# Performance work log

Measured on AMD Instinct MI355X. Metric: run time of the kernel, lower is better.

Reference implementation:

```python
import jax, jax.numpy as jnp
import numpy as np

K = 4
V = 32000
H = 512
B = 16
SOS = 1
EOS = 2


def setup_inputs() -> dict:
    key = jax.random.key(0)
    ks = jax.random.split(key, 8)
    s = 0.08  # small init keeps GRU/log_softmax well-conditioned
    return {
        "enc_h": jax.random.normal(ks[0], (B, H), jnp.float32),
        "E": jax.random.normal(ks[1], (V, H), jnp.float32) * s,
        "W_ih": jax.random.normal(ks[2], (H, 3 * H), jnp.float32) * s,
        "W_hh": jax.random.normal(ks[3], (H, 3 * H), jnp.float32) * s,
        "b_ih": jax.random.normal(ks[4], (3 * H,), jnp.float32) * s,
        "b_hh": jax.random.normal(ks[5], (3 * H,), jnp.float32) * s,
        "Wo": jax.random.normal(ks[6], (H, V), jnp.float32) * s,
        "bo": jax.random.normal(ks[7], (V,), jnp.float32) * s,
        "max_length": 32,
    }


def _beam_search(enc_h, E, W_ih, W_hh, b_ih, b_hh, Wo, bo, T):
    BK = B * K
    pos = jnp.arange(B, dtype=jnp.int32) * K  # pos_index
    # torch .repeat beam inflation: tiled layout (index i -> original i % B)
    h0 = jnp.tile(enc_h, (K, 1))  # [BK, H]
    inp0 = jnp.full((BK,), SOS, dtype=jnp.int32)
    ss0 = jnp.full((BK,), -jnp.inf, dtype=enc_h.dtype).at[pos].set(0.0)

    def gru(x, h):
        gi = x @ W_ih + b_ih
        gh = h @ W_hh + b_hh
        ir, iz, inn = jnp.split(gi, 3, axis=-1)
        hr, hz, hn = jnp.split(gh, 3, axis=-1)
        r = jax.nn.sigmoid(ir + hr)
        z = jax.nn.sigmoid(iz + hz)
        n = jnp.tanh(inn + r * hn)
        return (1.0 - z) * n + z * h

    def fwd_step(carry, _):
        inp, h, ss = carry
        h_new = gru(E[inp], h)                                   # [BK, H]
        logp = jax.nn.log_softmax(h_new @ Wo + bo, axis=-1)      # [BK, V]
        total = (ss[:, None] + logp).reshape(B, K * V)
        scores, cand = jax.lax.top_k(total, K)                   # [B, K]
        symbols = (cand % V).astype(jnp.int32).reshape(-1)       # input_var
        preds = (cand // V + pos[:, None]).astype(jnp.int32).reshape(-1)
        h_sel = h_new[preds]                                     # index_select hidden
        ss_new = scores.reshape(-1)
        ss_masked = jnp.where(symbols == EOS, -jnp.inf, ss_new)  # EOS masking
        return (symbols, h_sel, ss_masked), (logp, ss_new, preds, symbols, h_sel)

    _, (logps, step_scores, preds, syms, hiddens) = jax.lax.scan(
        fwd_step, (inp0, h0, ss0), None, length=T)

    # ---------------- backtrack ----------------
    last = step_scores[-1].reshape(B, K)
    s0, sorted_idx = jax.lax.top_k(last, K)
    tpred0 = (sorted_idx.astype(jnp.int32) + pos[:, None]).reshape(-1)
    lens0 = jnp.full((B, K), T, dtype=jnp.int32)
    hn0 = jnp.zeros((BK, H), dtype=enc_h.dtype)
    eos0 = jnp.zeros((B,), dtype=jnp.int32)

    def bt_step(carry, xs):
        tpred, eosf, s, lens, hn = carry
        logp_t, hid_t, pred_t, sym_t, score_t, tt = xs
        cur_out = logp_t[tpred]
        cur_hid = hid_t[tpred]
        cur_sym = sym_t[tpred]
        new_pred = pred_t[tpred]
        eos = sym_t == EOS
        eos_bk = eos.reshape(B, K).astype(jnp.int32)
        # original loop processes eos hits in descending beam order per batch
        higher = jnp.cumsum(eos_bk[:, ::-1], axis=1)[:, ::-1] - eos_bk
        occ = eosf[:, None] + higher
        res_k = K - occ % K - 1
        res_flat = (pos[:, None] + res_k).reshape(-1)
        idx = jnp.where(eos, res_flat, BK)  # BK = out of bounds -> dropped
        new_pred = new_pred.at[idx].set(pred_t, mode='drop')
        cur_out = cur_out.at[idx].set(logp_t, mode='drop')
        cur_hid = cur_hid.at[idx].set(hid_t, mode='drop')
        hn = hn.at[idx].set(hid_t, mode='drop')
        cur_sym = cur_sym.at[idx].set(sym_t, mode='drop')
        s = s.reshape(-1).at[idx].set(score_t, mode='drop').reshape(B, K)
        lens = lens.reshape(-1).at[idx].set(tt + 1, mode='drop').reshape(B, K)
        eosf = eosf + eos_bk.sum(axis=1)
        return (new_pred, eosf, s, lens, hn), (cur_out, cur_sym)

    ts = jnp.arange(T - 1, -1, -1, dtype=jnp.int32)
    (_, _, s_fin, lens_fin, hn_fin), (outs_rev, syms_rev) = jax.lax.scan(
        bt_step, (tpred0, eos0, s0, lens0, hn0),
        (logps[::-1], hiddens[::-1], preds[::-1], syms[::-1], step_scores[::-1], ts))

    s_sorted, re_idx = jax.lax.top_k(s_fin, K)
    lens_sorted = jnp.take_along_axis(lens_fin, re_idx, axis=1)
    re_flat = (re_idx.astype(jnp.int32) + pos[:, None]).reshape(-1)
    outs = outs_rev[::-1][:, re_flat].reshape(T, B, K, V)
    seqs = syms_rev[::-1][:, re_flat].reshape(T, B, K)
    decoder_outputs = outs[:, :, 0, :]            # [T, B, V]
    decoder_hidden = hn_fin[re_flat].reshape(B, K, H)[:, 0, :]
    return decoder_outputs, decoder_hidden, s_sorted, lens_sorted, seqs


def reference(enc_h, E, W_ih, W_hh, b_ih, b_hh, Wo, bo, max_length):
    return _beam_search(enc_h, E, W_ih, W_hh, b_ih, b_hh, Wo, bo, int(max_length))
```

## Files before the change

### kernel.cpp

```cpp
#include <hip/hip_runtime.h>
#include <math.h>
#include <limits.h>

#define T_STEPS 32
#define BATCH   16
#define KBEAM   4
#define BKR     64
#define HD      512
#define VOC     32000
#define G3      1536
#define SOS_TOK 1
#define EOS_TOK 2
#define NSP     (VOC/64)
#define NE      (NSP*4)
#define NBG     (G3/64)
#define FMBL    2

#define OFF_HCUR   ((size_t)0)
#define OFF_GBUF   (OFF_HCUR + (size_t)BKR*HD)
#define OFF_HNEW   (OFF_GBUF + (size_t)2*BKR*G3)
#define OFF_LSE    (OFF_HNEW + (size_t)T_STEPS*BKR*HD)
#define OFF_SS     (OFF_LSE + (size_t)T_STEPS*BKR)
#define OFF_SCORES (OFF_SS + BKR)
#define OFF_HNFIN  (OFF_SCORES + (size_t)T_STEPS*BKR)
#define OFF_PV     (OFF_HNFIN + (size_t)BKR*HD)
#define OFF_PM     (OFF_PV + (size_t)BKR*NE)
#define OFF_PS     (OFF_PM + (size_t)BKR*NSP)
#define OFF_FEND   (OFF_PS + (size_t)BKR*NSP)
#define IOFF_INP    0
#define IOFF_PREDS  64
#define IOFF_SYMS   (IOFF_PREDS + T_STEPS*BKR)
#define IOFF_RMAP   (IOFF_SYMS + T_STEPS*BKR)
#define IOFF_PC     (IOFF_RMAP + T_STEPS*BATCH)
#define IOFF_END    (IOFF_PC + BKR*NE)
#define S_WOH   ((size_t)0)
#define S_WOL   (S_WOH + (size_t)NSP*16*2048)
#define S_WGH   (S_WOL + (size_t)NSP*16*2048)
#define S_WGL   (S_WGH + (size_t)2*NBG*16*2048)
#define S_HNH   (S_WGL + (size_t)2*NBG*16*2048)
#define S_HNL   (S_HNH + (size_t)T_STEPS*BKR*HD)
#define S_HCH   (S_HNL + (size_t)T_STEPS*BKR*HD)
#define S_HCL   (S_HCH + (size_t)BKR*HD)
#define S_EIH   (S_HCL + (size_t)BKR*HD)
#define S_EIL   (S_EIH + (size_t)BKR*HD)
#define S_END   (S_EIL + (size_t)BKR*HD)

#define O_HID  ((size_t)T_STEPS*BATCH*VOC)
#define O_SSRT (O_HID + (size_t)BATCH*HD)
#define O_LENS (O_SSRT + BATCH*KBEAM)
#define O_SEQS (O_LENS + BATCH*KBEAM)

typedef short bf16x8 __attribute__((ext_vector_type(8)));
typedef float f32x4  __attribute__((ext_vector_type(4)));

#define TSZ 2560

__device__ __forceinline__ unsigned short f2bf(float x){
    unsigned u = __float_as_uint(x);
    return (unsigned short)((u + 0x7fffu + ((u >> 16) & 1u)) >> 16);
}
__device__ __forceinline__ float bf2f(unsigned short h){
    return __uint_as_float(((unsigned)h) << 16);
}

__device__ __forceinline__ void dump_C(f32x4 (&acc)[4], float (*Cs)[65], int wave, int lane){
    #pragma unroll
    for (int g = 0; g < 4; ++g){
// ... 3 lines not shown
        for (int r = 0; r < 4; ++r) Cs[row + r][col] = acc[g][r];
    }
}

__device__ __forceinline__ void ins4(float* bv, int* bc, float s, int c){
    bool g0 = (s > bv[0]) || (s == bv[0] && c < bc[0]);
    bool g1 = (s > bv[1]) || (s == bv[1] && c < bc[1]);
    bool g2 = (s > bv[2]) || (s == bv[2] && c < bc[2]);
    bool g3 = (s > bv[3]) || (s == bv[3] && c < bc[3]);
    if (g0){ bv[3]=bv[2];bc[3]=bc[2]; bv[2]=bv[1];bc[2]=bc[1]; bv[1]=bv[0];bc[1]=bc[0]; bv[0]=s; bc[0]=c; }
    else if (g1){ bv[3]=bv[2];bc[3]=bc[2]; bv[2]=bv[1];bc[2]=bc[1]; bv[1]=s; bc[1]=c; }
    else if (g2){ bv[3]=bv[2];bc[3]=bc[2]; bv[2]=s; bc[2]=c; }
    else if (g3){ bv[3]=s; bc[3]=c; }
}


__global__ __launch_bounds__(256) void prepack_kernel(const float* __restrict__ W, int N,
    unsigned short* __restrict__ oh, unsigned short* __restrict__ ol)
{
    const int bx = blockIdx.x, kt = blockIdx.y, tid = threadIdx.x;
    const int bn = tid >> 2, kq = (tid & 3) * 8;
    union { unsigned short u[8]; uint4 v; } h8, l8;
    #pragma unroll
    for (int j = 0; j < 8; ++j){
        float x = W[(size_t)(kt*32 + kq + j) * (size_t)N + bx*64 + bn];
        unsigned short h = f2bf(x);
        h8.u[j] = h; l8.u[j] = f2bf(x - bf2f(h));
    }
    const size_t base = ((size_t)bx*16 + kt) * 2048 + (size_t)tid * 8;
    *(uint4*)(oh + base) = h8.v;
    *(uint4*)(ol + base) = l8.v;
}


__global__ __launch_bounds__(256) void gates_pre_kernel(
    const unsigned short* __restrict__ eih, const unsigned short* __restrict__ eil,
    const unsigned short* __restrict__ hch, const unsigned short* __restrict__ hcl,
    const unsigned short* __restrict__ wgh, const unsigned short* __restrict__ wgl,
    const float* __restrict__ b_ih, const float* __restrict__ b_hh,
    float* __restrict__ gbuf)
{
    __shared__ __align__(16) unsigned short sm[2*4*TSZ];
    const int z = blockIdx.y, bx = blockIdx.x, n0 = bx * 64;
    const int tid = threadIdx.x;
    const unsigned short* ahg = z ? hch : eih;
    const unsigned short* alg = z ? hcl : eil;
    const size_t bt = ((size_t)z*NBG + bx) * 16 * 2048;
    const unsigned short* bth = wgh + bt;
    const unsigned short* btl = wgl + bt;
    const int row = tid >> 2, kq = (tid & 3) * 8;
    const int wave = tid >> 6, lane = tid & 63;
    const int fr = lane & 15, fq = lane >> 4;
    const int wr = row * 40 + kq;
    f32x4 acc[4];
    #pragma unroll
    for (int g = 0; g < 4; ++g) acc[g] = (f32x4){0.f,0.f,0.f,0.f};
    {
        uint4 a_h = *(const uint4*)(ahg + (size_t)row*512 + kq);
        uint4 a_l = *(const uint4*)(alg + (size_t)row*512 + kq);
        uint4 b_h = *(const uint4*)(bth + (size_t)tid*8);
        uint4 b_l = *(const uint4*)(btl + (size_t)tid*8);
        *(uint4*)(sm + 0*TSZ + wr) = a_h;
        *(uint4*)(sm + 1*TSZ + wr) = a_l;
        *(uint4*)(sm + 2*TSZ + wr) = b_h;
        *(uint4*)(sm + 3*TSZ + wr) = b_l;
    }
    __syncthreads();
    #pragma unroll 2
    for (int kt = 0; kt < 16; ++kt){
        unsigned short* cb = sm + (kt & 1) * (4*TSZ);
        unsigned short* nb = sm + ((kt & 1) ^ 1) * (4*TSZ);
        uint4 a_h, a_l, b_h, b_l;
        if (kt < 15){
            a_h = *(const uint4*)(ahg + (size_t)row*512 + (kt+1)*32 + kq);
            a_l = *(const uint4*)(alg + (size_t)row*512 + (kt+1)*32 + kq);
            b_h = *(const uint4*)(bth + (size_t)(kt+1)*2048 + (size_t)tid*8);
            b_l = *(const uint4*)(btl + (size_t)(kt+1)*2048 + (size_t)tid*8);
        }
        bf16x8 bh = *(const bf16x8*)(cb + 2*TSZ + (wave*16 + fr)*40 + fq*8);
        bf16x8 bl = *(const bf16x8*)(cb + 3*TSZ + (wave*16 + fr)*40 + fq*8);
        #pragma unroll
        for (int g = 0; g < 4; ++g){
            bf16x8 ah = *(const bf16x8*)(cb + 0*TSZ + (g*16 + fr)*40 + fq*8);
            bf16x8 al = *(const bf16x8*)(cb + 1*TSZ + (g*16 + fr)*40 + fq*8);
            acc[g] = __builtin_amdgcn_mfma_f32_16x16x32_bf16(ah, bh, acc[g], 0, 0, 0);
            acc[g] = __builtin_amdgcn_mfma_f32_16x16x32_bf16(ah, bl, acc[g], 0, 0, 0);
            acc[g] = __builtin_amdgcn_mfma_f32_16x16x32_bf16(al, bh, acc[g], 0, 0, 0);
        }
        if (kt < 15){
            *(uint4*)(nb + 0*TSZ + wr) = a_h;
            *(uint4*)(nb + 1*TSZ + wr) = a_l;
            *(uint4*)(nb + 2*TSZ + wr) = b_h;
            *(uint4*)(nb + 3*TSZ + wr) = b_l;
        }
        __syncthreads();
    }
    const float* bias = z ? b_hh : b_ih;
    const int col = wave*16 + fr;
    const float bz = bias[n0 + col];
    float* gp = gbuf + (size_t)z * BKR * G3 + n0 + col;
    #pragma unroll
    for (int g = 0; g < 4; ++g){
        const int r0 = g*16 + fq*4;
        #pragma unroll
        for (int r = 0; r < 4; ++r)
            gp[(size_t)(r0 + r) * G3] = acc[g][r] + bz;
    }
}

__global__ __launch_bounds__(256) void logits_pre_kernel(
    const unsigned short* __restrict__ hnh, const unsigned short* __restrict__ hnl,
    const unsigned short* __restrict__ woh, const unsigned short* __restrict__ wol,
    const float* __restrict__ bo,
    float* __restrict__ pv, int* __restrict__ pc, float* __restrict__ pm, float* __restrict__ ps)
{
    __shared__ __align__(16) unsigned short sm[2*4*TSZ];
    const int bx = blockIdx.x, n0 = bx * 64;
    const int tid = threadIdx.x;
    const unsigned short* bth = woh + (size_t)bx * 16 * 2048;
    const unsigned short* btl = wol + (size_t)bx * 16 * 2048;
    const int row = tid >> 2, kq = (tid & 3) * 8;
    const int wave = tid >> 6, lane = tid & 63;
    const int fr = lane & 15, fq = lane >> 4;
    const int wr = row * 40 + kq;
    f32x4 acc[4];
    #pragma unroll
    for (int g = 0; g < 4; ++g) acc[g] = (f32x4){0.f,0.f,0.f,0.f};
    {
        uint4 a_h = *(const uint4*)(hnh + (size_t)row*512 + kq);
        uint4 a_l = *(const uint4*)(hnl + (size_t)row*512 + kq);
        uint4 b_h = *(const uint4*)(bth + (size_t)tid*8);
        uint4 b_l = *(const uint4*)(btl + (size_t)tid*8);
        *(uint4*)(sm + 0*TSZ + wr) = a_h;
        *(uint4*)(sm + 1*TSZ + wr) = a_l;
        *(uint4*)(sm + 2*TSZ + wr) = b_h;
        *(uint4*)(sm + 3*TSZ + wr) = b_l;
    }
    __syncthreads();
    #pragma unroll 2
    for (int kt = 0; kt < 16; ++kt){
        unsigned short* cb = sm + (kt & 1) * (4*TSZ);
        unsigned short* nb = sm + ((kt & 1) ^ 1) * (4*TSZ);
        uint4 a_h, a_l, b_h, b_l;
        if (kt < 15){
            a_h = *(const uint4*)(hnh + (size_t)row*512 + (kt+1)*32 + kq);
            a_l = *(const uint4*)(hnl + (size_t)row*512 + (kt+1)*32 + kq);
            b_h = *(const uint4*)(bth + (size_t)(kt+1)*2048 + (size_t)tid*8);
            b_l = *(const uint4*)(btl + (size_t)(kt+1)*2048 + (size_t)tid*8);
        }
        bf16x8 bh = *(const bf16x8*)(cb + 2*TSZ + (wave*16 + fr)*40 + fq*8);
        bf16x8 bl = *(const bf16x8*)(cb + 3*TSZ + (wave*16 + fr)*40 + fq*8);
        #pragma unroll
        for (int g = 0; g < 4; ++g){
            bf16x8 ah = *(const bf16x8*)(cb + 0*TSZ + (g*16 + fr)*40 + fq*8);
            bf16x8 al = *(const bf16x8*)(cb + 1*TSZ + (g*16 + fr)*40 + fq*8);
            acc[g] = __builtin_amdgcn_mfma_f32_16x16x32_bf16(ah, bh, acc[g], 0, 0, 0);
            acc[g] = __builtin_amdgcn_mfma_f32_16x16x32_bf16(ah, bl, acc[g], 0, 0, 0);
            acc[g] = __builtin_amdgcn_mfma_f32_16x16x32_bf16(al, bh, acc[g], 0, 0, 0);
        }
        if (kt < 15){
            *(uint4*)(nb + 0*TSZ + wr) = a_h;
            *(uint4*)(nb + 1*TSZ + wr) = a_l;
            *(uint4*)(nb + 2*TSZ + wr) = b_h;
            *(uint4*)(nb + 3*TSZ + wr) = b_l;
        }
        __syncthreads();
    }
    float (*Cs)[65] = (float(*)[65])sm;
    dump_C(acc, Cs, wave, lane);
    __syncthreads();
    const int c0 = (tid & 3) * 16;
    float bv[4] = {-INFINITY,-INFINITY,-INFINITY,-INFINITY};
    int bc[4] = {INT_MAX, INT_MAX, INT_MAX, INT_MAX};
    float m = -INFINITY, s = 0.f;
    #pragma unroll
    for (int j = 0; j < 16; ++j){
        float x = Cs[row][c0 + j] + bo[n0 + c0 + j];
        if (x > m){ s = s * expf(m - x) + 1.f; m = x; }
        else s += expf(x - m);
        ins4(bv, bc, x, n0 + c0 + j);
    }
    #pragma unroll
    for (int o = 1; o < 4; o <<= 1){
        float ov[4]; int oc[4];
        #pragma unroll
        for (int q = 0; q < 4; ++q){ ov[q] = __shfl_xor(bv[q], o); oc[q] = __shfl_xor(bc[q], o); }
        #pragma unroll
        for (int q = 0; q < 4; ++q) ins4(bv, bc, ov[q], oc[q]);
        float m2 = __shfl_xor(m, o), s2 = __shfl_xor(s, o);
        float M = fmaxf(m, m2);
        s = s * expf(m - M) + s2 * expf(m2 - M);
        m = M;
    }
    if ((tid & 3) == 0){
        const size_t base = (size_t)row * NE + (size_t)bx * 4;
        #pragma unroll
        for (int q = 0; q < 4; ++q){ pv[base + q] = bv[q]; pc[base + q] = bc[q]; }
        pm[row * NSP + bx] = m; ps[row * NSP + bx] = s;
    }
}

__global__ __launch_bounds__(256) void final_pre_kernel(
    const unsigned short* __restrict__ hnh, const unsigned short* __restrict__ hnl,
    const int* __restrict__ rmap, const float* __restrict__ lse_all,
    const unsigned short* __restrict__ woh, const unsigned short* __restrict__ wol,
    const float* __restrict__ bo, float* __restrict__ out)
{
    __shared__ __align__(16) unsigned short sm[2*6*TSZ];
    __shared__ int sidx[64*FMBL]; __shared__ float subm[64*FMBL];
    const int tid = threadIdx.x;
    const int bx = blockIdx.x, n0 = bx * 64;
    const int mbase = blockIdx.y * (64 * FMBL);
    if (tid < 64*FMBL){ int g = rmap[mbase + tid]; sidx[tid] = g; subm[tid] = lse_all[g]; }
    __syncthreads();
    const int row = tid >> 2, kq = (tid & 3) * 8;
    const int wave = tid >> 6, lane = tid & 63;
    const int fr = lane & 15, fq = lane >> 4;
    const int wr = row * 40 + kq;
    const size_t r0 = (size_t)sidx[row] * 512;
    const size_t r1 = (size_t)sidx[64 + row] * 512;
    const unsigned short* bth = woh + (size_t)bx * 16 * 2048;
    const unsigned short* btl = wol + (size_t)bx * 16 * 2048;
    f32x4 acc[FMBL][4];
    #pragma unroll
    for (int mb = 0; mb < FMBL; ++mb)
        #pragma unroll
        for (int g = 0; g < 4; ++g) acc[mb][g] = (f32x4){0.f,0.f,0.f,0.f};
    {
        uint4 a0h = *(const uint4*)(hnh + r0 + kq);
        uint4 a0l = *(const uint4*)(hnl + r0 + kq);
        uint4 a1h = *(const uint4*)(hnh + r1 + kq);
        uint4 a1l = *(const uint4*)(hnl + r1 + kq);
        uint4 b_h = *(const uint4*)(bth + (size_t)tid*8);
        uint4 b_l = *(const uint4*)(btl + (size_t)tid*8);
        *(uint4*)(sm + 0*TSZ + wr) = a0h;
        *(uint4*)(sm + 1*TSZ + wr) = a0l;
        *(uint4*)(sm + 2*TSZ + wr) = a1h;
        *(uint4*)(sm + 3*TSZ + wr) = a1l;
        *(uint4*)(sm + 4*TSZ + wr) = b_h;
        *(uint4*)(sm + 5*TSZ + wr) = b_l;
    }
    __syncthreads();
    #pragma unroll 2
    for (int kt = 0; kt < 16; ++kt){
        unsigned short* cb = sm + (kt & 1) * (6*TSZ);
        unsigned short* nb = sm + ((kt & 1) ^ 1) * (6*TSZ);
        uint4 a0h, a0l, a1h, a1l, b_h, b_l;
        if (kt < 15){
            a0h = *(const uint4*)(hnh + r0 + (kt+1)*32 + kq);
            a0l = *(const uint4*)(hnl + r0 + (kt+1)*32 + kq);
            a1h = *(const uint4*)(hnh + r1 + (kt+1)*32 + kq);
            a1l = *(const uint4*)(hnl + r1 + (kt+1)*32 + kq);
            b_h = *(const uint4*)(bth + (size_t)(kt+1)*2048 + (size_t)tid*8);
            b_l = *(const uint4*)(btl + (size_t)(kt+1)*2048 + (size_t)tid*8);
        }
        bf16x8 bh = *(const bf16x8*)(cb + 4*TSZ + (wave*16 + fr)*40 + fq*8);
        bf16x8 bl = *(const bf16x8*)(cb + 5*TSZ + (wave*16 + fr)*40 + fq*8);
        #pragma unroll
        for (int mb = 0; mb < FMBL; ++mb){
            #pragma unroll
            for (int g = 0; g < 4; ++g){
                bf16x8 ah = *(const bf16x8*)(cb + (2*mb+0)*TSZ + (g*16 + fr)*40 + fq*8);
                bf16x8 al = *(const bf16x8*)(cb + (2*mb+1)*TSZ + (g*16 + fr)*40 + fq*8);
                acc[mb][g] = __builtin_amdgcn_mfma_f32_16x16x32_bf16(ah, bh, acc[mb][g], 0, 0, 0);
                acc[mb][g] = __builtin_amdgcn_mfma_f32_16x16x32_bf16(ah, bl, acc[mb][g], 0, 0, 0);
                acc[mb][g] = __builtin_amdgcn_mfma_f32_16x16x32_bf16(al, bh, acc[mb][g], 0, 0, 0);
            }
        }
        if (kt < 15){
            *(uint4*)(nb + 0*TSZ + wr) = a0h;
            *(uint4*)(nb + 1*TSZ + wr) = a0l;
            *(uint4*)(nb + 2*TSZ + wr) = a1h;
            *(uint4*)(nb + 3*TSZ + wr) = a1l;
            *(uint4*)(nb + 4*TSZ + wr) = b_h;
            *(uint4*)(nb + 5*TSZ + wr) = b_l;
        }
        __syncthreads();
    }
    const int col = n0 + wave*16 + fr;
    const float bz = bo[col];
    #pragma unroll
    for (int mb = 0; mb < FMBL; ++mb){
        #pragma unroll
        for (int g = 0; g < 4; ++g){
            const int rb = mb*64 + g*16 + fq*4;
            #pragma unroll
            for (int r = 0; r < 4; ++r){
                const int rowi = rb + r;
                out[(size_t)(mbase + rowi) * VOC + col] = acc[mb][g][r] + bz - subm[rowi];
            }
        }
    }
}

__device__ __forceinline__ void mfma_core(
    const float* __restrict__ Abase, const int* __restrict__ ridx, int mbase,
    const float* __restrict__ B, int ldb, int n0,
    unsigned short (&Ah)[64][40], unsigned short (&Al)[64][40],
    unsigned short (&Bh)[64][40], unsigned short (&Bl)[64][40],
    int (&sidx)[64], f32x4 (&acc)[4])
{
    const int tid = threadIdx.x;
    if (tid < 64) sidx[tid] = ridx ? ridx[mbase + tid] : (mbase + tid);
    #pragma unroll
    for (int g = 0; g < 4; ++g) acc[g] = (f32x4){0.f, 0.f, 0.f, 0.f};
    const int wave = tid >> 6, lane = tid & 63;
    const int am = tid >> 2, ak0 = (tid & 3) * 8;
    const int bn = tid & 63, br0 = (tid >> 6) * 8;
    __syncthreads();
    const float* bcol = B + n0 + bn;
// ... 234 lines not shown
        }
        #pragma unroll
        for (int u = 0; u < KBEAM; ++u){
            int cand = gc[u]; float val = gv[u];
            int sym = cand % VOC; int pg = b * KBEAM + cand / VOC;
            int slot = b * KBEAM + u;
            scores_all[t * BKR + slot] = val;
            syms_all[t * BKR + slot] = sym;
            preds_all[t * BKR + slot] = pg;
            ss[slot] = (sym == EOS_TOK) ? -INFINITY : val;
            inp[slot] = sym;
            spred[u] = pg; ssym[u] = sym;
        }
    }
    __syncthreads();
    for (int x = tid; x < KBEAM * HD; x += 256){
        int u = x >> 9, j = x & 511;
        const int idx = (b * KBEAM + u) * HD + j;
        float v = h_new[spred[u] * HD + j];
        h_cur[idx] = v;
        if (hch){
            unsigned short h = f2bf(v);
            hch[idx] = h; hcl[idx] = f2bf(v - bf2f(h));
            float e = E[(size_t)ssym[u] * HD + j];
            unsigned short eh = f2bf(e);
            eih[idx] = eh; eil[idx] = f2bf(e - bf2f(eh));
        }
    }
}

__global__ void init_kernel(const float* __restrict__ enc_h, const float* __restrict__ E,
    float* __restrict__ h_cur, float* __restrict__ ss, int* __restrict__ inp,
    unsigned short* __restrict__ hch, unsigned short* __restrict__ hcl,
    unsigned short* __restrict__ eih, unsigned short* __restrict__ eil)
{
    const int i = blockIdx.x;
    for (int j = threadIdx.x; j < HD; j += blockDim.x){
        float v = enc_h[(i & (BATCH - 1)) * HD + j];
        h_cur[i * HD + j] = v;
        if (hch){
            const int idx = i * HD + j;
            unsigned short h = f2bf(v);
            hch[idx] = h; hcl[idx] = f2bf(v - bf2f(h));
            float e = E[(size_t)SOS_TOK * HD + j];
            unsigned short eh = f2bf(e);
            eih[idx] = eh; eil[idx] = f2bf(e - bf2f(eh));
        }
    }
    if (i == 0 && threadIdx.x < BKR){
        ss[threadIdx.x] = ((threadIdx.x & (KBEAM - 1)) == 0) ? 0.f : -INFINITY;
        inp[threadIdx.x] = SOS_TOK;
    }
}

__global__ __launch_bounds__(256) void backtrack_kernel(
    const float* __restrict__ scores_all, const int* __restrict__ preds_all, const int* __restrict__ syms_all,
    const float* __restrict__ h_new_all, float* __restrict__ hn_fin,
    int* __restrict__ rmap, float* __restrict__ out)
{
    __shared__ int   l_syms[T_STEPS*BKR];
    __shared__ int   l_preds[T_STEPS*BKR];
    __shared__ float l_scores[T_STEPS*BKR];
    __shared__ int   outrow_s[T_STEPS*BKR];
    __shared__ int   cursym_s[T_STEPS*BKR];
    __shared__ int tpred[64]; __shared__ float sfin[64]; __shared__ int lensq[64];
    __shared__ int eosf[BATCH];
    __shared__ int orow[64], csym[64], npred_s[64];
    __shared__ int cp_slot[64], cp_src[64]; __shared__ int nc_b[BATCH];
    __shared__ int reidx[64];
    const int tid = threadIdx.x;

    for (int x = tid; x < T_STEPS*BKR; x += 256){
        l_syms[x]   = syms_all[x];
        l_preds[x]  = preds_all[x];
        l_scores[x] = scores_all[x];
    }
    for (int x = tid; x < BKR*HD; x += 256) hn_fin[x] = 0.f;
    __syncthreads();

    if (tid < BATCH){
        const int b = tid;
        float v[KBEAM]; int used[KBEAM];
        #pragma unroll
        for (int k = 0; k < KBEAM; ++k){ v[k] = l_scores[(T_STEPS-1)*BKR + b*KBEAM + k]; used[k] = 0; }
// ... 98 lines not shown
}

extern "C" void kernel_launch(void* const* d_in, const int* in_sizes, int n_in,
                              void* d_out, int out_size, void* d_ws, size_t ws_size,
                              hipStream_t stream)
{
    const float* enc_h = (const float*)d_in[0];
    const float* E     = (const float*)d_in[1];
    const float* W_ih  = (const float*)d_in[2];
    const float* W_hh  = (const float*)d_in[3];
    const float* b_ih  = (const float*)d_in[4];
    const float* b_hh  = (const float*)d_in[5];
    const float* Wo    = (const float*)d_in[6];
    const float* bo    = (const float*)d_in[7];
    float* out = (float*)d_out;

    float* w = (float*)d_ws;
    float* h_cur      = w + OFF_HCUR;
    float* gbuf       = w + OFF_GBUF;
    float* h_new_all  = w + OFF_HNEW;
    float* lse_all    = w + OFF_LSE;
    float* ss         = w + OFF_SS;
    float* scores_all = w + OFF_SCORES;
    float* hn_fin     = w + OFF_HNFIN;
    float* pv         = w + OFF_PV;
    float* pm         = w + OFF_PM;
    float* ps         = w + OFF_PS;
    int* wi         = (int*)(w + OFF_FEND);
    int* inp        = wi + IOFF_INP;
    int* preds_all  = wi + IOFF_PREDS;
    int* syms_all   = wi + IOFF_SYMS;
    int* rmap       = wi + IOFF_RMAP;
    int* pc         = wi + IOFF_PC;
    unsigned short* sb = (unsigned short*)(wi + IOFF_END);
    unsigned short* woh = sb + S_WOH;
    unsigned short* wol = sb + S_WOL;
    unsigned short* wgh = sb + S_WGH;
    unsigned short* wgl = sb + S_WGL;
    unsigned short* hnh = sb + S_HNH;
    unsigned short* hnl = sb + S_HNL;
    unsigned short* hch = sb + S_HCH;
    unsigned short* hcl = sb + S_HCL;
    unsigned short* eih = sb + S_EIH;
    unsigned short* eil = sb + S_EIL;

    const size_t NEED = (size_t)OFF_FEND*4 + (size_t)IOFF_END*4 + (size_t)S_END*2;
    const bool pre = (ws_size >= NEED);

    init_kernel<<<dim3(BKR), 256, 0, stream>>>(enc_h, E, h_cur, ss, inp,
        pre ? hch : nullptr, hcl, eih, eil);
    if (pre){
        prepack_kernel<<<dim3(NSP, 16), 256, 0, stream>>>(Wo, VOC, woh, wol);
        prepack_kernel<<<dim3(NBG, 16), 256, 0, stream>>>(W_ih, G3, wgh, wgl);
        prepack_kernel<<<dim3(NBG, 16), 256, 0, stream>>>(W_hh, G3,
            wgh + (size_t)NBG*16*2048, wgl + (size_t)NBG*16*2048);
    }
    for (int t = 0; t < T_STEPS; ++t){
        float* h_new_t = h_new_all + (size_t)t * BKR * HD;
        unsigned short* hnh_t = hnh + (size_t)t * BKR * HD;
        unsigned short* hnl_t = hnl + (size_t)t * BKR * HD;
        if (pre){
            gates_pre_kernel<<<dim3(NBG, 2), 256, 0, stream>>>(eih, eil, hch, hcl,
                wgh, wgl, b_ih, b_hh, gbuf);
        } else {
            gates_mfma_kernel<<<dim3(NBG, 2), 256, 0, stream>>>(E, inp, h_cur, W_ih, W_hh, b_ih, b_hh, gbuf);
        }
        gru_combine_kernel<<<dim3(BKR*HD/256), 256, 0, stream>>>(gbuf, h_cur, h_new_t,
            pre ? hnh_t : nullptr, hnl_t);
        if (pre){
            logits_pre_kernel<<<dim3(NSP), 256, 0, stream>>>(hnh_t, hnl_t, woh, wol, bo, pv, pc, pm, ps);
        } else {
            logits_topk_kernel<<<dim3(NSP), 256, 0, stream>>>(h_new_t, Wo, bo, pv, pc, pm, ps);
        }
        topk_phase_b<<<dim3(BATCH), 256, 0, stream>>>(pv, pc, pm, ps, t, scores_all, preds_all, syms_all,
            ss, inp, lse_all, h_new_t, h_cur, E,
            pre ? hch : nullptr, hcl, eih, eil);
    }
    backtrack_kernel<<<dim3(1), 256, 0, stream>>>(scores_all, preds_all, syms_all, h_new_all, hn_fin,
                                                  rmap, out);
    if (pre){
        final_pre_kernel<<<dim3(NSP, (T_STEPS*BATCH)/(64*FMBL)), 256, 0, stream>>>(
            hnh, hnl, rmap, lse_all, woh, wol, bo, out);
    } else {
        final_mfma_kernel<<<dim3(NSP, T_STEPS*BATCH/64), 256, 0, stream>>>(h_new_all, rmap, lse_all, Wo, bo, out);
    }
}
```

Measured before the change: 2.619 ms.

## Fuse GRU combine and beam top-k into last-arriving blocks via atomic counters

Per-step counters let the last blocks to finish the gates kernel do the GRU combine. Likewise, the last blocks of the logits kernel do the per-batch top-k merge, beam selection and hidden/embedding gather. This removes two kernel launches per decode step, 64 in total, and the launch gaps that come with them. In exchange it relies on spin-waiting on global atomics, assumes all blocks of a grid make progress, and leaves only 8 or 16 blocks doing the tail work. It also swaps the grid axes of the final projection kernel so that blocks sharing the same weight tile run next to each other.

```diff
diff --git a/kernel.cpp b/kernel.cpp
--- a/kernel.cpp
+++ b/kernel.cpp
@@ -32,7 +32,9 @@
 #define IOFF_SYMS   (IOFF_PREDS + T_STEPS*BKR)
 #define IOFF_RMAP   (IOFF_SYMS + T_STEPS*BKR)
 #define IOFF_PC     (IOFF_RMAP + T_STEPS*BATCH)
-#define IOFF_END    (IOFF_PC + BKR*NE)
+#define IOFF_GCNT   (IOFF_PC + BKR*NE)
+#define IOFF_LCNT   (IOFF_GCNT + T_STEPS)
+#define IOFF_END    (IOFF_LCNT + T_STEPS)
 #define S_WOH   ((size_t)0)
 #define S_WOL   (S_WOH + (size_t)NSP*16*2048)
 #define S_WGH   (S_WOL + (size_t)NSP*16*2048)
@@ -102,13 +104,15 @@
     *(uint4*)(ol + base) = l8.v;
 }
 
-
 __global__ __launch_bounds__(256) void gates_pre_kernel(
     const unsigned short* __restrict__ eih, const unsigned short* __restrict__ eil,
     const unsigned short* __restrict__ hch, const unsigned short* __restrict__ hcl,
     const unsigned short* __restrict__ wgh, const unsigned short* __restrict__ wgl,
     const float* __restrict__ b_ih, const float* __restrict__ b_hh,
-    float* __restrict__ gbuf)
+    float* __restrict__ gbuf,
+    const float* __restrict__ h_cur, float* __restrict__ h_new,
+    unsigned short* __restrict__ hnh, unsigned short* __restrict__ hnl,
+    int* __restrict__ gcnt)
 {
     __shared__ __align__(16) unsigned short sm[2*4*TSZ];
     const int z = blockIdx.y, bx = blockIdx.x, n0 = bx * 64;
@@ -176,13 +180,53 @@
         for (int r = 0; r < 4; ++r)
             gp[(size_t)(r0 + r) * G3] = acc[g][r] + bz;
     }
+    __syncthreads();
+    int* comm = (int*)sm;
+    if (tid == 0){
+        __threadfence();
+        comm[0] = atomicAdd(gcnt, 1);
+    }
+    __syncthreads();
+    const int old = comm[0];
+    if (old >= 2*NBG - 8 && old < 2*NBG){
+        if (tid == 0){
+            while (__hip_atomic_load(gcnt, __ATOMIC_ACQUIRE, __HIP_MEMORY_SCOPE_AGENT) < 2*NBG)
+                __builtin_amdgcn_s_sleep(1);
+        }
+        __syncthreads();
+        __threadfence();
+        const int slice = old - (2*NBG - 8);
+        for (int x = tid; x < 64*64; x += 256){
+            const int rr = x >> 6, j = (slice << 6) + (x & 63);
+            const int xi = rr * HD + j;
+            const float* gi = gbuf + (size_t)rr * G3;
+            const float* gh = gbuf + (size_t)BKR * G3 + (size_t)rr * G3;
+            float ir = gi[j], iz = gi[j + 512], inn = gi[j + 1024];
+            float hr = gh[j], hz = gh[j + 512], hnv = gh[j + 1024];
+            float r  = 1.f / (1.f + expf(-(ir + hr)));
+            float zz = 1.f / (1.f + expf(-(iz + hz)));
+            float n  = tanhf(inn + r * hnv);
+            float v = (1.f - zz) * n + zz * h_cur[xi];
+            h_new[xi] = v;
+            unsigned short h = f2bf(v);
+            hnh[xi] = h; hnl[xi] = f2bf(v - bf2f(h));
+        }
+    }
 }
 
 __global__ __launch_bounds__(256) void logits_pre_kernel(
     const unsigned short* __restrict__ hnh, const unsigned short* __restrict__ hnl,
     const unsigned short* __restrict__ woh, const unsigned short* __restrict__ wol,
     const float* __restrict__ bo,
-    float* __restrict__ pv, int* __restrict__ pc, float* __restrict__ pm, float* __restrict__ ps)
+    float* __restrict__ pv, int* __restrict__ pc, float* __restrict__ pm, float* __restrict__ ps,
+    int t,
+    float* __restrict__ scores_all, int* __restrict__ preds_all, int* __restrict__ syms_all,
+    float* __restrict__ ss, int* __restrict__ inp, float* __restrict__ lse_all,
+    const float* __restrict__ h_new, float* __restrict__ h_cur,
+    const float* __restrict__ E,
+    unsigned short* __restrict__ hch, unsigned short* __restrict__ hcl,
+    unsigned short* __restrict__ eih, unsigned short* __restrict__ eil,
+    int* __restrict__ lcnt)
 {
     __shared__ __align__(16) unsigned short sm[2*4*TSZ];
     const int bx = blockIdx.x, n0 = bx * 64;
@@ -239,34 +283,134 @@
     float (*Cs)[65] = (float(*)[65])sm;
     dump_C(acc, Cs, wave, lane);
     __syncthreads();
-    const int c0 = (tid & 3) * 16;
-    float bv[4] = {-INFINITY,-INFINITY,-INFINITY,-INFINITY};
-    int bc[4] = {INT_MAX, INT_MAX, INT_MAX, INT_MAX};
-    float m = -INFINITY, s = 0.f;
-    #pragma unroll
-    for (int j = 0; j < 16; ++j){
-        float x = Cs[row][c0 + j] + bo[n0 + c0 + j];
-        if (x > m){ s = s * expf(m - x) + 1.f; m = x; }
-        else s += expf(x - m);
-        ins4(bv, bc, x, n0 + c0 + j);
-    }
-    #pragma unroll
-    for (int o = 1; o < 4; o <<= 1){
-        float ov[4]; int oc[4];
-        #pragma unroll
-        for (int q = 0; q < 4; ++q){ ov[q] = __shfl_xor(bv[q], o); oc[q] = __shfl_xor(bc[q], o); }
-        #pragma unroll
-        for (int q = 0; q < 4; ++q) ins4(bv, bc, ov[q], oc[q]);
-        float m2 = __shfl_xor(m, o), s2 = __shfl_xor(s, o);
-        float M = fmaxf(m, m2);
-        s = s * expf(m - M) + s2 * expf(m2 - M);
-        m = M;
-    }
-    if ((tid & 3) == 0){
-        const size_t base = (size_t)row * NE + (size_t)bx * 4;
-        #pragma unroll
-        for (int q = 0; q < 4; ++q){ pv[base + q] = bv[q]; pc[base + q] = bc[q]; }
-        pm[row * NSP + bx] = m; ps[row * NSP + bx] = s;
+    {
+        const int c0 = (tid & 3) * 16;
+        float bv[4] = {-INFINITY,-INFINITY,-INFINITY,-INFINITY};
+        int bc[4] = {INT_MAX, INT_MAX, INT_MAX, INT_MAX};
+        float m = -INFINITY, s = 0.f;
+        #pragma unroll
+        for (int j = 0; j < 16; ++j){
+            float x = Cs[row][c0 + j] + bo[n0 + c0 + j];
+            if (x > m){ s = s * expf(m - x) + 1.f; m = x; }
+            else s += expf(x - m);
+            ins4(bv, bc, x, n0 + c0 + j);
+        }
+        #pragma unroll
+        for (int o = 1; o < 4; o <<= 1){
+            float ov[4]; int oc[4];
+            #pragma unroll
+            for (int q = 0; q < 4; ++q){ ov[q] = __shfl_xor(bv[q], o); oc[q] = __shfl_xor(bc[q], o); }
+            #pragma unroll
+            for (int q = 0; q < 4; ++q) ins4(bv, bc, ov[q], oc[q]);
+            float m2 = __shfl_xor(m, o), s2 = __shfl_xor(s, o);
+            float M = fmaxf(m, m2);
+            s = s * expf(m - M) + s2 * expf(m2 - M);
+            m = M;
+        }
+        if ((tid & 3) == 0){
+            const size_t base = (size_t)row * NE + (size_t)bx * 4;
+            #pragma unroll
+            for (int q = 0; q < 4; ++q){ pv[base + q] = bv[q]; pc[base + q] = bc[q]; }
+            pm[row * NSP + bx] = m; ps[row * NSP + bx] = s;
+        }
+    }
+    __syncthreads();
+    unsigned char* smb = (unsigned char*)sm;
+    int* comm = (int*)(smb + 20480);
+    if (tid == 0){
+        __threadfence();
+        comm[0] = atomicAdd(lcnt, 1);
+    }
+    __syncthreads();
+    const int old = comm[0];
+    if (old >= NSP - BATCH && old < NSP){
+        if (tid == 0){
+            while (__hip_atomic_load(lcnt, __ATOMIC_ACQUIRE, __HIP_MEMORY_SCOPE_AGENT) < NSP)
+                __builtin_amdgcn_s_sleep(1);
+        }
+        __syncthreads();
+        __threadfence();
+        const int b = old - (NSP - BATCH);
+        float (*rtv)[4] = (float(*)[4])(smb + 20544);
+        int   (*rtc)[4] = (int(*)[4])(smb + 20608);
+        float* rlse = (float*)(smb + 20672);
+        int* spred = (int*)(smb + 20688);
+        int* ssym  = (int*)(smb + 20704);
+        const int rrow = b * KBEAM + wave;
+        float bv[4] = {-INFINITY,-INFINITY,-INFINITY,-INFINITY};
+        int bc[4] = {INT_MAX, INT_MAX, INT_MAX, INT_MAX};
+        for (int e = lane; e < NE; e += 64)
+            ins4(bv, bc, pv[(size_t)rrow * NE + e], pc[(size_t)rrow * NE + e]);
+        #pragma unroll
+        for (int o = 1; o < 64; o <<= 1){
+            float ov[4]; int oc[4];
+            #pragma unroll
+            for (int q = 0; q < 4; ++q){ ov[q] = __shfl_xor(bv[q], o); oc[q] = __shfl_xor(bc[q], o); }
+            #pragma unroll
+            for (int q = 0; q < 4; ++q) ins4(bv, bc, ov[q], oc[q]);
+        }
+        float m = -INFINITY, s = 0.f;
+        for (int e = lane; e < NSP; e += 64){
+            float m2 = pm[rrow * NSP + e], s2 = ps[rrow * NSP + e];
+            float M = fmaxf(m, m2);
+            s = s * expf(m - M) + s2 * expf(m2 - M);
+            m = M;
+        }
+        #pragma unroll
+        for (int o = 1; o < 64; o <<= 1){
+            float m2 = __shfl_xor(m, o), s2 = __shfl_xor(s, o);
+            float M = fmaxf(m, m2);
+            s = s * expf(m - M) + s2 * expf(m2 - M);
+            m = M;
+        }
+        if (lane == 0){
+            #pragma unroll
+            for (int q = 0; q < 4; ++q){ rtv[wave][q] = bv[q]; rtc[wave][q] = bc[q]; }
+            rlse[wave] = m + logf(s);
+        }
+        __syncthreads();
+        if (tid == 0){
+            float gv[4] = {-INFINITY,-INFINITY,-INFINITY,-INFINITY};
+            int gc[4] = {INT_MAX, INT_MAX, INT_MAX, INT_MAX};
+            #pragma unroll
+            for (int kl = 0; kl < KBEAM; ++kl){
+                const int r2 = b * KBEAM + kl;
+                float lse = rlse[kl];
+                lse_all[t * BKR + r2] = lse;
+                float off = ss[r2] - lse;
+                if (off == -INFINITY){
+                    #pragma unroll
+                    for (int q = 0; q < 4; ++q) ins4(gv, gc, -INFINITY, kl * VOC + q);
+                } else {
+                    #pragma unroll
+                    for (int q = 0; q < 4; ++q) ins4(gv, gc, rtv[kl][q] + off, kl * VOC + rtc[kl][q]);
+                }
+            }
+            #pragma unroll
+            for (int u = 0; u < KBEAM; ++u){
+                int cand = gc[u]; float val = gv[u];
+                int sym = cand % VOC; int pg = b * KBEAM + cand / VOC;
+                int slot = b * KBEAM + u;
+                scores_all[t * BKR + slot] = val;
+                syms_all[t * BKR + slot] = sym;
+                preds_all[t * BKR + slot] = pg;
+                ss[slot] = (sym == EOS_TOK) ? -INFINITY : val;
+                inp[slot] = sym;
+                spred[u] = pg; ssym[u] = sym;
+            }
+        }
+        __syncthreads();
+        for (int x = tid; x < KBEAM * HD; x += 256){
+            int u = x >> 9, j = x & 511;
+            const int idx = (b * KBEAM + u) * HD + j;
+            float v = h_new[spred[u] * HD + j];
+            h_cur[idx] = v;
+            unsigned short h = f2bf(v);
+            hch[idx] = h; hcl[idx] = f2bf(v - bf2f(h));
+            float e = E[(size_t)ssym[u] * HD + j];
+            unsigned short eh = f2bf(e);
+            eih[idx] = eh; eil[idx] = f2bf(e - bf2f(eh));
+        }
     }
 }
 
@@ -279,8 +423,8 @@
     __shared__ __align__(16) unsigned short sm[2*6*TSZ];
     __shared__ int sidx[64*FMBL]; __shared__ float subm[64*FMBL];
     const int tid = threadIdx.x;
-    const int bx = blockIdx.x, n0 = bx * 64;
-    const int mbase = blockIdx.y * (64 * FMBL);
+    const int bx = blockIdx.y, n0 = bx * 64;
+    const int mbase = blockIdx.x * (64 * FMBL);
     if (tid < 64*FMBL){ int g = rmap[mbase + tid]; sidx[tid] = g; subm[tid] = lse_all[g]; }
     __syncthreads();
     const int row = tid >> 2, kq = (tid & 3) * 8;
@@ -646,7 +790,8 @@
 __global__ void init_kernel(const float* __restrict__ enc_h, const float* __restrict__ E,
     float* __restrict__ h_cur, float* __restrict__ ss, int* __restrict__ inp,
     unsigned short* __restrict__ hch, unsigned short* __restrict__ hcl,
-    unsigned short* __restrict__ eih, unsigned short* __restrict__ eil)
+    unsigned short* __restrict__ eih, unsigned short* __restrict__ eil,
+    int* __restrict__ cnts)
 {
     const int i = blockIdx.x;
     for (int j = threadIdx.x; j < HD; j += blockDim.x){
@@ -664,6 +809,9 @@
     if (i == 0 && threadIdx.x < BKR){
         ss[threadIdx.x] = ((threadIdx.x & (KBEAM - 1)) == 0) ? 0.f : -INFINITY;
         inp[threadIdx.x] = SOS_TOK;
+    }
+    if (i == 1 && cnts){
+        for (int x = threadIdx.x; x < 2*T_STEPS; x += blockDim.x) cnts[x] = 0;
     }
 }
 
@@ -828,6 +976,8 @@
     int* syms_all   = wi + IOFF_SYMS;
     int* rmap       = wi + IOFF_RMAP;
     int* pc         = wi + IOFF_PC;
+    int* gcnt       = wi + IOFF_GCNT;
+    int* lcnt       = wi + IOFF_LCNT;
     unsigned short* sb = (unsigned short*)(wi + IOFF_END);
     unsigned short* woh = sb + S_WOH;
     unsigned short* wol = sb + S_WOL;
@@ -844,7 +994,7 @@
     const bool pre = (ws_size >= NEED);
 
     init_kernel<<<dim3(BKR), 256, 0, stream>>>(enc_h, E, h_cur, ss, inp,
-        pre ? hch : nullptr, hcl, eih, eil);
+        pre ? hch : nullptr, hcl, eih, eil, pre ? gcnt : nullptr);
     if (pre){
         prepack_kernel<<<dim3(NSP, 16), 256, 0, stream>>>(Wo, VOC, woh, wol);
         prepack_kernel<<<dim3(NBG, 16), 256, 0, stream>>>(W_ih, G3, wgh, wgl);
@@ -857,25 +1007,24 @@
         unsigned short* hnl_t = hnl + (size_t)t * BKR * HD;
         if (pre){
             gates_pre_kernel<<<dim3(NBG, 2), 256, 0, stream>>>(eih, eil, hch, hcl,
-                wgh, wgl, b_ih, b_hh, gbuf);
+                wgh, wgl, b_ih, b_hh, gbuf, h_cur, h_new_t, hnh_t, hnl_t, gcnt + t);
+            logits_pre_kernel<<<dim3(NSP), 256, 0, stream>>>(hnh_t, hnl_t, woh, wol, bo,
+                pv, pc, pm, ps, t, scores_all, preds_all, syms_all, ss, inp, lse_all,
+                h_new_t, h_cur, E, hch, hcl, eih, eil, lcnt + t);
         } else {
             gates_mfma_kernel<<<dim3(NBG, 2), 256, 0, stream>>>(E, inp, h_cur, W_ih, W_hh, b_ih, b_hh, gbuf);
-        }
-        gru_combine_kernel<<<dim3(BKR*HD/256), 256, 0, stream>>>(gbuf, h_cur, h_new_t,
-            pre ? hnh_t : nullptr, hnl_t);
-        if (pre){
-            logits_pre_kernel<<<dim3(NSP), 256, 0, stream>>>(hnh_t, hnl_t, woh, wol, bo, pv, pc, pm, ps);
-        } else {
+            gru_combine_kernel<<<dim3(BKR*HD/256), 256, 0, stream>>>(gbuf, h_cur, h_new_t,
+                nullptr, hnl_t);
             logits_topk_kernel<<<dim3(NSP), 256, 0, stream>>>(h_new_t, Wo, bo, pv, pc, pm, ps);
-        }
-        topk_phase_b<<<dim3(BATCH), 256, 0, stream>>>(pv, pc, pm, ps, t, scores_all, preds_all, syms_all,
-            ss, inp, lse_all, h_new_t, h_cur, E,
-            pre ? hch : nullptr, hcl, eih, eil);
+            topk_phase_b<<<dim3(BATCH), 256, 0, stream>>>(pv, pc, pm, ps, t, scores_all, preds_all, syms_all,
+                ss, inp, lse_all, h_new_t, h_cur, E,
+                nullptr, hcl, eih, eil);
+        }
     }
     backtrack_kernel<<<dim3(1), 256, 0, stream>>>(scores_all, preds_all, syms_all, h_new_all, hn_fin,
                                                   rmap, out);
     if (pre){
-        final_pre_kernel<<<dim3(NSP, (T_STEPS*BATCH)/(64*FMBL)), 256, 0, stream>>>(
+        final_pre_kernel<<<dim3((T_STEPS*BATCH)/(64*FMBL), NSP), 256, 0, stream>>>(
             hnh, hnl, rmap, lse_all, woh, wol, bo, out);
     } else {
         final_mfma_kernel<<<dim3(NSP, T_STEPS*BATCH/64), 256, 0, stream>>>(h_new_all, rmap, lse_all, Wo, bo, out);
```

Result: slower. 3.624 ms (+38.4%).

## Fuse GRU combine into gates kernel via last-blocks counter; deepen global prefetch

Applied to the files above, without the earlier changes.

The GRU elementwise combine is folded into the gates GEMM kernel. An atomic arrival counter lets the last eight arriving blocks spin until all 48 blocks have written their gates, then each computes a 64-column slice of the new hidden state and its bf16 hi/lo split, removing one launch per step. The GEMM loops in the gates, logits and final kernels now prefetch global tiles two iterations ahead instead of one, at the cost of more registers. The final kernel's grid axes are swapped so that consecutive blocks share the same weight tile. The spin-wait assumes all 48 blocks are co-resident, which holds for this small grid.

```diff
diff --git a/kernel.cpp b/kernel.cpp
--- a/kernel.cpp
+++ b/kernel.cpp
@@ -32,7 +32,9 @@
 #define IOFF_SYMS   (IOFF_PREDS + T_STEPS*BKR)
 #define IOFF_RMAP   (IOFF_SYMS + T_STEPS*BKR)
 #define IOFF_PC     (IOFF_RMAP + T_STEPS*BATCH)
-#define IOFF_END    (IOFF_PC + BKR*NE)
+#define IOFF_GCNT   (IOFF_PC + BKR*NE)
+#define IOFF_LCNT   (IOFF_GCNT + T_STEPS)
+#define IOFF_END    (IOFF_LCNT + T_STEPS)
 #define S_WOH   ((size_t)0)
 #define S_WOL   (S_WOH + (size_t)NSP*16*2048)
 #define S_WGH   (S_WOL + (size_t)NSP*16*2048)
@@ -102,13 +104,15 @@
     *(uint4*)(ol + base) = l8.v;
 }
 
-
 __global__ __launch_bounds__(256) void gates_pre_kernel(
     const unsigned short* __restrict__ eih, const unsigned short* __restrict__ eil,
     const unsigned short* __restrict__ hch, const unsigned short* __restrict__ hcl,
     const unsigned short* __restrict__ wgh, const unsigned short* __restrict__ wgl,
     const float* __restrict__ b_ih, const float* __restrict__ b_hh,
-    float* __restrict__ gbuf)
+    float* __restrict__ gbuf,
+    const float* __restrict__ h_cur, float* __restrict__ h_new,
+    unsigned short* __restrict__ hnh, unsigned short* __restrict__ hnl,
+    int* __restrict__ gcnt)
 {
     __shared__ __align__(16) unsigned short sm[2*4*TSZ];
     const int z = blockIdx.y, bx = blockIdx.x, n0 = bx * 64;
@@ -135,17 +139,21 @@
         *(uint4*)(sm + 2*TSZ + wr) = b_h;
         *(uint4*)(sm + 3*TSZ + wr) = b_l;
     }
+    uint4 pa_h = *(const uint4*)(ahg + (size_t)row*512 + 32 + kq);
+    uint4 pa_l = *(const uint4*)(alg + (size_t)row*512 + 32 + kq);
+    uint4 pb_h = *(const uint4*)(bth + 2048 + (size_t)tid*8);
+    uint4 pb_l = *(const uint4*)(btl + 2048 + (size_t)tid*8);
     __syncthreads();
     #pragma unroll 2
     for (int kt = 0; kt < 16; ++kt){
         unsigned short* cb = sm + (kt & 1) * (4*TSZ);
-        unsigned short* nb = sm + ((kt & 1) ^ 1) * (4*TSZ);
-        uint4 a_h, a_l, b_h, b_l;
-        if (kt < 15){
-            a_h = *(const uint4*)(ahg + (size_t)row*512 + (kt+1)*32 + kq);
-            a_l = *(const uint4*)(alg + (size_t)row*512 + (kt+1)*32 + kq);
-            b_h = *(const uint4*)(bth + (size_t)(kt+1)*2048 + (size_t)tid*8);
-            b_l = *(const uint4*)(btl + (size_t)(kt+1)*2048 + (size_t)tid*8);
+        unsigned short* nbuf = sm + ((kt & 1) ^ 1) * (4*TSZ);
+        uint4 na_h = pa_h, na_l = pa_l, nb_h = pb_h, nb_l = pb_l;
+        if (kt < 14){
+            na_h = *(const uint4*)(ahg + (size_t)row*512 + (kt+2)*32 + kq);
+            na_l = *(const uint4*)(alg + (size_t)row*512 + (kt+2)*32 + kq);
+            nb_h = *(const uint4*)(bth + (size_t)(kt+2)*2048 + (size_t)tid*8);
+            nb_l = *(const uint4*)(btl + (size_t)(kt+2)*2048 + (size_t)tid*8);
         }
         bf16x8 bh = *(const bf16x8*)(cb + 2*TSZ + (wave*16 + fr)*40 + fq*8);
         bf16x8 bl = *(const bf16x8*)(cb + 3*TSZ + (wave*16 + fr)*40 + fq*8);
@@ -158,12 +166,13 @@
             acc[g] = __builtin_amdgcn_mfma_f32_16x16x32_bf16(al, bh, acc[g], 0, 0, 0);
         }
         if (kt < 15){
-            *(uint4*)(nb + 0*TSZ + wr) = a_h;
-            *(uint4*)(nb + 1*TSZ + wr) = a_l;
-            *(uint4*)(nb + 2*TSZ + wr) = b_h;
-            *(uint4*)(nb + 3*TSZ + wr) = b_l;
+            *(uint4*)(nbuf + 0*TSZ + wr) = pa_h;
+            *(uint4*)(nbuf + 1*TSZ + wr) = pa_l;
+            *(uint4*)(nbuf + 2*TSZ + wr) = pb_h;
+            *(uint4*)(nbuf + 3*TSZ + wr) = pb_l;
         }
         __syncthreads();
+        pa_h = na_h; pa_l = na_l; pb_h = nb_h; pb_l = nb_l;
     }
     const float* bias = z ? b_hh : b_ih;
     const int col = wave*16 + fr;
@@ -175,6 +184,38 @@
         #pragma unroll
         for (int r = 0; r < 4; ++r)
             gp[(size_t)(r0 + r) * G3] = acc[g][r] + bz;
+    }
+    __syncthreads();
+    int* comm = (int*)sm;
+    if (tid == 0){
+        __threadfence();
+        comm[0] = atomicAdd(gcnt, 1);
+    }
+    __syncthreads();
+    const int old = comm[0];
+    if (old >= 2*NBG - 8 && old < 2*NBG){
+        if (tid == 0){
+            while (__hip_atomic_load(gcnt, __ATOMIC_ACQUIRE, __HIP_MEMORY_SCOPE_AGENT) < 2*NBG)
+                __builtin_amdgcn_s_sleep(1);
+        }
+        __syncthreads();
+        __threadfence();
+        const int slice = old - (2*NBG - 8);
+        for (int x = tid; x < 64*64; x += 256){
+            const int rr = x >> 6, j = (slice << 6) + (x & 63);
+            const int xi = rr * HD + j;
+            const float* gi = gbuf + (size_t)rr * G3;
+            const float* gh = gbuf + (size_t)BKR * G3 + (size_t)rr * G3;
+            float ir = gi[j], iz = gi[j + 512], inn = gi[j + 1024];
+            float hr = gh[j], hz = gh[j + 512], hnv = gh[j + 1024];
+            float r  = 1.f / (1.f + expf(-(ir + hr)));
+            float zz = 1.f / (1.f + expf(-(iz + hz)));
+            float n  = tanhf(inn + r * hnv);
+            float v = (1.f - zz) * n + zz * h_cur[xi];
+            h_new[xi] = v;
+            unsigned short h = f2bf(v);
+            hnh[xi] = h; hnl[xi] = f2bf(v - bf2f(h));
+        }
     }
 }
 
@@ -206,17 +247,21 @@
         *(uint4*)(sm + 2*TSZ + wr) = b_h;
         *(uint4*)(sm + 3*TSZ + wr) = b_l;
     }
+    uint4 pa_h = *(const uint4*)(hnh + (size_t)row*512 + 32 + kq);
+    uint4 pa_l = *(const uint4*)(hnl + (size_t)row*512 + 32 + kq);
+    uint4 pb_h = *(const uint4*)(bth + 2048 + (size_t)tid*8);
+    uint4 pb_l = *(const uint4*)(btl + 2048 + (size_t)tid*8);
     __syncthreads();
     #pragma unroll 2
     for (int kt = 0; kt < 16; ++kt){
         unsigned short* cb = sm + (kt & 1) * (4*TSZ);
-        unsigned short* nb = sm + ((kt & 1) ^ 1) * (4*TSZ);
-        uint4 a_h, a_l, b_h, b_l;
-        if (kt < 15){
-            a_h = *(const uint4*)(hnh + (size_t)row*512 + (kt+1)*32 + kq);
-            a_l = *(const uint4*)(hnl + (size_t)row*512 + (kt+1)*32 + kq);
-            b_h = *(const uint4*)(bth + (size_t)(kt+1)*2048 + (size_t)tid*8);
-            b_l = *(const uint4*)(btl + (size_t)(kt+1)*2048 + (size_t)tid*8);
+        unsigned short* nbuf = sm + ((kt & 1) ^ 1) * (4*TSZ);
+        uint4 na_h = pa_h, na_l = pa_l, nb_h = pb_h, nb_l = pb_l;
+        if (kt < 14){
+            na_h = *(const uint4*)(hnh + (size_t)row*512 + (kt+2)*32 + kq);
+            na_l = *(const uint4*)(hnl + (size_t)row*512 + (kt+2)*32 + kq);
+            nb_h = *(const uint4*)(bth + (size_t)(kt+2)*2048 + (size_t)tid*8);
+            nb_l = *(const uint4*)(btl + (size_t)(kt+2)*2048 + (size_t)tid*8);
         }
         bf16x8 bh = *(const bf16x8*)(cb + 2*TSZ + (wave*16 + fr)*40 + fq*8);
         bf16x8 bl = *(const bf16x8*)(cb + 3*TSZ + (wave*16 + fr)*40 + fq*8);
@@ -229,12 +274,13 @@
             acc[g] = __builtin_amdgcn_mfma_f32_16x16x32_bf16(al, bh, acc[g], 0, 0, 0);
         }
         if (kt < 15){
-            *(uint4*)(nb + 0*TSZ + wr) = a_h;
-            *(uint4*)(nb + 1*TSZ + wr) = a_l;
-            *(uint4*)(nb + 2*TSZ + wr) = b_h;
-            *(uint4*)(nb + 3*TSZ + wr) = b_l;
+            *(uint4*)(nbuf + 0*TSZ + wr) = pa_h;
+            *(uint4*)(nbuf + 1*TSZ + wr) = pa_l;
+            *(uint4*)(nbuf + 2*TSZ + wr) = pb_h;
+            *(uint4*)(nbuf + 3*TSZ + wr) = pb_l;
         }
         __syncthreads();
+        pa_h = na_h; pa_l = na_l; pb_h = nb_h; pb_l = nb_l;
     }
     float (*Cs)[65] = (float(*)[65])sm;
     dump_C(acc, Cs, wave, lane);
@@ -279,8 +325,8 @@
     __shared__ __align__(16) unsigned short sm[2*6*TSZ];
     __shared__ int sidx[64*FMBL]; __shared__ float subm[64*FMBL];
     const int tid = threadIdx.x;
-    const int bx = blockIdx.x, n0 = bx * 64;
-    const int mbase = blockIdx.y * (64 * FMBL);
+    const int bx = blockIdx.y, n0 = bx * 64;
+    const int mbase = blockIdx.x * (64 * FMBL);
     if (tid < 64*FMBL){ int g = rmap[mbase + tid]; sidx[tid] = g; subm[tid] = lse_all[g]; }
     __syncthreads();
     const int row = tid >> 2, kq = (tid & 3) * 8;
@@ -310,19 +356,25 @@
         *(uint4*)(sm + 4*TSZ + wr) = b_h;
         *(uint4*)(sm + 5*TSZ + wr) = b_l;
     }
+    uint4 p0h = *(const uint4*)(hnh + r0 + 32 + kq);
+    uint4 p0l = *(const uint4*)(hnl + r0 + 32 + kq);
+    uint4 p1h = *(const uint4*)(hnh + r1 + 32 + kq);
+    uint4 p1l = *(const uint4*)(hnl + r1 + 32 + kq);
+    uint4 pbh = *(const uint4*)(bth + 2048 + (size_t)tid*8);
+    uint4 pbl = *(const uint4*)(btl + 2048 + (size_t)tid*8);
     __syncthreads();
     #pragma unroll 2
     for (int kt = 0; kt < 16; ++kt){
         unsigned short* cb = sm + (kt & 1) * (6*TSZ);
-        unsigned short* nb = sm + ((kt & 1) ^ 1) * (6*TSZ);
-        uint4 a0h, a0l, a1h, a1l, b_h, b_l;
-        if (kt < 15){
-            a0h = *(const uint4*)(hnh + r0 + (kt+1)*32 + kq);
-            a0l = *(const uint4*)(hnl + r0 + (kt+1)*32 + kq);
-            a1h = *(const uint4*)(hnh + r1 + (kt+1)*32 + kq);
-            a1l = *(const uint4*)(hnl + r1 + (kt+1)*32 + kq);
-            b_h = *(const uint4*)(bth + (size_t)(kt+1)*2048 + (size_t)tid*8);
-            b_l = *(const uint4*)(btl + (size_t)(kt+1)*2048 + (size_t)tid*8);
+        unsigned short* nbuf = sm + ((kt & 1) ^ 1) * (6*TSZ);
+        uint4 n0h = p0h, n0l = p0l, n1h = p1h, n1l = p1l, nbh = pbh, nbl = pbl;
+        if (kt < 14){
+            n0h = *(const uint4*)(hnh + r0 + (kt+2)*32 + kq);
+            n0l = *(const uint4*)(hnl + r0 + (kt+2)*32 + kq);
+            n1h = *(const uint4*)(hnh + r1 + (kt+2)*32 + kq);
+            n1l = *(const uint4*)(hnl + r1 + (kt+2)*32 + kq);
+            nbh = *(const uint4*)(bth + (size_t)(kt+2)*2048 + (size_t)tid*8);
+            nbl = *(const uint4*)(btl + (size_t)(kt+2)*2048 + (size_t)tid*8);
         }
         bf16x8 bh = *(const bf16x8*)(cb + 4*TSZ + (wave*16 + fr)*40 + fq*8);
         bf16x8 bl = *(const bf16x8*)(cb + 5*TSZ + (wave*16 + fr)*40 + fq*8);
@@ -338,14 +390,15 @@
             }
         }
         if (kt < 15){
-            *(uint4*)(nb + 0*TSZ + wr) = a0h;
-            *(uint4*)(nb + 1*TSZ + wr) = a0l;
-            *(uint4*)(nb + 2*TSZ + wr) = a1h;
-            *(uint4*)(nb + 3*TSZ + wr) = a1l;
-            *(uint4*)(nb + 4*TSZ + wr) = b_h;
-            *(uint4*)(nb + 5*TSZ + wr) = b_l;
+            *(uint4*)(nbuf + 0*TSZ + wr) = p0h;
+            *(uint4*)(nbuf + 1*TSZ + wr) = p0l;
+            *(uint4*)(nbuf + 2*TSZ + wr) = p1h;
+            *(uint4*)(nbuf + 3*TSZ + wr) = p1l;
+            *(uint4*)(nbuf + 4*TSZ + wr) = pbh;
+            *(uint4*)(nbuf + 5*TSZ + wr) = pbl;
         }
         __syncthreads();
+        p0h = n0h; p0l = n0l; p1h = n1h; p1l = n1l; pbh = nbh; pbl = nbl;
     }
     const int col = n0 + wave*16 + fr;
     const float bz = bo[col];
@@ -646,7 +699,8 @@
 __global__ void init_kernel(const float* __restrict__ enc_h, const float* __restrict__ E,
     float* __restrict__ h_cur, float* __restrict__ ss, int* __restrict__ inp,
     unsigned short* __restrict__ hch, unsigned short* __restrict__ hcl,
-    unsigned short* __restrict__ eih, unsigned short* __restrict__ eil)
+    unsigned short* __restrict__ eih, unsigned short* __restrict__ eil,
+    int* __restrict__ cnts)
 {
     const int i = blockIdx.x;
     for (int j = threadIdx.x; j < HD; j += blockDim.x){
@@ -664,6 +718,9 @@
     if (i == 0 && threadIdx.x < BKR){
         ss[threadIdx.x] = ((threadIdx.x & (KBEAM - 1)) == 0) ? 0.f : -INFINITY;
         inp[threadIdx.x] = SOS_TOK;
+    }
+    if (i == 1 && cnts){
+        for (int x = threadIdx.x; x < 2*T_STEPS; x += blockDim.x) cnts[x] = 0;
     }
 }
 
@@ -828,6 +885,7 @@
     int* syms_all   = wi + IOFF_SYMS;
     int* rmap       = wi + IOFF_RMAP;
     int* pc         = wi + IOFF_PC;
+    int* gcnt       = wi + IOFF_GCNT;
     unsigned short* sb = (unsigned short*)(wi + IOFF_END);
     unsigned short* woh = sb + S_WOH;
     unsigned short* wol = sb + S_WOL;
@@ -844,7 +902,7 @@
     const bool pre = (ws_size >= NEED);
 
     init_kernel<<<dim3(BKR), 256, 0, stream>>>(enc_h, E, h_cur, ss, inp,
-        pre ? hch : nullptr, hcl, eih, eil);
+        pre ? hch : nullptr, hcl, eih, eil, pre ? gcnt : nullptr);
     if (pre){
         prepack_kernel<<<dim3(NSP, 16), 256, 0, stream>>>(Wo, VOC, woh, wol);
         prepack_kernel<<<dim3(NBG, 16), 256, 0, stream>>>(W_ih, G3, wgh, wgl);
@@ -857,25 +915,26 @@
         unsigned short* hnl_t = hnl + (size_t)t * BKR * HD;
         if (pre){
             gates_pre_kernel<<<dim3(NBG, 2), 256, 0, stream>>>(eih, eil, hch, hcl,
-                wgh, wgl, b_ih, b_hh, gbuf);
+                wgh, wgl, b_ih, b_hh, gbuf, h_cur, h_new_t, hnh_t, hnl_t, gcnt + t);
+            logits_pre_kernel<<<dim3(NSP), 256, 0, stream>>>(hnh_t, hnl_t, woh, wol, bo,
+                pv, pc, pm, ps);
+            topk_phase_b<<<dim3(BATCH), 256, 0, stream>>>(pv, pc, pm, ps, t, scores_all, preds_all, syms_all,
+                ss, inp, lse_all, h_new_t, h_cur, E,
+                hch, hcl, eih, eil);
         } else {
             gates_mfma_kernel<<<dim3(NBG, 2), 256, 0, stream>>>(E, inp, h_cur, W_ih, W_hh, b_ih, b_hh, gbuf);
-        }
-        gru_combine_kernel<<<dim3(BKR*HD/256), 256, 0, stream>>>(gbuf, h_cur, h_new_t,
-            pre ? hnh_t : nullptr, hnl_t);
-        if (pre){
-            logits_pre_kernel<<<dim3(NSP), 256, 0, stream>>>(hnh_t, hnl_t, woh, wol, bo, pv, pc, pm, ps);
-        } else {
+            gru_combine_kernel<<<dim3(BKR*HD/256), 256, 0, stream>>>(gbuf, h_cur, h_new_t,
+                nullptr, hnl_t);
             logits_topk_kernel<<<dim3(NSP), 256, 0, stream>>>(h_new_t, Wo, bo, pv, pc, pm, ps);
-        }
-        topk_phase_b<<<dim3(BATCH), 256, 0, stream>>>(pv, pc, pm, ps, t, scores_all, preds_all, syms_all,
-            ss, inp, lse_all, h_new_t, h_cur, E,
-            pre ? hch : nullptr, hcl, eih, eil);
+            topk_phase_b<<<dim3(BATCH), 256, 0, stream>>>(pv, pc, pm, ps, t, scores_all, preds_all, syms_all,
+                ss, inp, lse_all, h_new_t, h_cur, E,
+                nullptr, hcl, eih, eil);
+        }
     }
     backtrack_kernel<<<dim3(1), 256, 0, stream>>>(scores_all, preds_all, syms_all, h_new_all, hn_fin,
                                                   rmap, out);
     if (pre){
-        final_pre_kernel<<<dim3(NSP, (T_STEPS*BATCH)/(64*FMBL)), 256, 0, stream>>>(
+        final_pre_kernel<<<dim3((T_STEPS*BATCH)/(64*FMBL), NSP), 256, 0, stream>>>(
             hnh, hnl, rmap, lse_all, woh, wol, bo, out);
     } else {
         final_mfma_kernel<<<dim3(NSP, T_STEPS*BATCH/64), 256, 0, stream>>>(h_new_all, rmap, lse_all, Wo, bo, out);
```

New measurement: 3.023 ms. 1.15x slower.
